# Kernel optimization log

Hardware: AMD Instinct MI355X
Metric: run time of the kernel (lower is better)

## Reference

```python
import jax, jax.numpy as jnp
import numpy as np
from jax import lax

SCALE = 1.0
SHIFT = 0.0
H = 1024
IN = 1024
B = 64
S = 512


def setup_inputs() -> dict:
    key = jax.random.key(0)
    ks = jax.random.split(key, 9)
    s_in = 1.0 / np.sqrt(IN)
    s_h = 1.0 / np.sqrt(H)
    return {
        "x": jax.random.normal(ks[0], (B, S, IN), jnp.float32),
        # layer 0: ih Linear(IN, 4H), hh Linear(H, 4H) — torch stores W as [out, in]
        "W_ih0": jax.random.uniform(ks[1], (4 * H, IN), jnp.float32, -s_in, s_in),
        "b_ih0": jax.random.uniform(ks[2], (4 * H,), jnp.float32, -s_in, s_in),
        "W_hh0": jax.random.uniform(ks[3], (4 * H, H), jnp.float32, -s_h, s_h),
        "b_hh0": jax.random.uniform(ks[4], (4 * H,), jnp.float32, -s_h, s_h),
        # layer 1: ih Linear(H, 4H), hh Linear(H, 4H)
        "W_ih1": jax.random.uniform(ks[5], (4 * H, H), jnp.float32, -s_h, s_h),
        "b_ih1": jax.random.uniform(ks[6], (4 * H,), jnp.float32, -s_h, s_h),
        "W_hh1": jax.random.uniform(ks[7], (4 * H, H), jnp.float32, -s_h, s_h),
        "b_hh1": jax.random.uniform(ks[8], (4 * H,), jnp.float32, -s_h, s_h),
    }


def _scaled_sigmoid(x):
    return SCALE * jax.nn.sigmoid(x) + SHIFT


def _lstm_layer(x_seq, W_ih, b_ih, W_hh, b_hh):
    """x_seq: (B, S, D). Returns (outputs (B,S,H), h_n (B,H), c_n (B,H))."""
    b = x_seq.shape[0]
    # precompute input projections for all timesteps: (S, B, 4H)
    xp = (jnp.einsum('bsd,gd->sbg', x_seq, W_ih) + b_ih).astype(x_seq.dtype)

    def step(carry, xp_t):
        h, c = carry
        gates = xp_t + h @ W_hh.T + b_hh  # (B, 4H)
        i_g, f_g, g_g, o_g = jnp.split(gates, 4, axis=-1)
        i = _scaled_sigmoid(i_g)
        f = _scaled_sigmoid(f_g)
        g = jnp.tanh(g_g)
        o = _scaled_sigmoid(o_g)
        c_next = f * c + i * g
        h_next = o * jnp.tanh(c_next)
        return (h_next, c_next), h_next

    h0 = jnp.zeros((b, W_hh.shape[1]), x_seq.dtype)
    c0 = jnp.zeros((b, W_hh.shape[1]), x_seq.dtype)
    (h_n, c_n), ys = lax.scan(step, (h0, c0), xp)
    return ys.transpose(1, 0, 2), h_n, c_n


def reference(x, W_ih0, b_ih0, W_hh0, b_hh0, W_ih1, b_ih1, W_hh1, b_hh1):
    out0, h0, c0 = _lstm_layer(x, W_ih0, b_ih0, W_hh0, b_hh0)
    out1, h1, c1 = _lstm_layer(out0, W_ih1, b_ih1, W_hh1, b_hh1)
    h_n = jnp.stack([h0, h1], axis=0)  # (num_layers, B, H)
    c_n = jnp.stack([c0, c1], axis=0)
    return out1, h_n, c_n
```

## Files before the change

### kernel.cpp

```cpp
#include <hip/hip_runtime.h>
#include <stdint.h>

typedef __attribute__((ext_vector_type(8))) short short8;
typedef __attribute__((ext_vector_type(4))) float f32x4;

#define MFMA16(a, b, c) __builtin_amdgcn_mfma_f32_16x16x32_bf16((a), (b), (c), 0, 0, 0)
#define AL(p) __hip_atomic_load((p), __ATOMIC_RELAXED, __HIP_MEMORY_SCOPE_AGENT)
#define AS(p, v) __hip_atomic_store((p), (v), __ATOMIC_RELAXED, __HIP_MEMORY_SCOPE_AGENT)

__device__ __forceinline__ unsigned short f2bf(float f) {
  unsigned u = __float_as_uint(f);
  u = (u + 0x7FFFu + ((u >> 16) & 1u)) >> 16;
  return (unsigned short)u;
}
__device__ __forceinline__ float bf2f(unsigned short u) {
  return __uint_as_float(((unsigned)u) << 16);
}

__global__ void k_prep(const float* __restrict__ x,
                       const float* __restrict__ w0, const float* __restrict__ w1,
                       const float* __restrict__ w2, const float* __restrict__ w3,
                       const float* __restrict__ a0, const float* __restrict__ b0,
                       const float* __restrict__ a1, const float* __restrict__ b1,
                       unsigned short* __restrict__ xbf,
                       unsigned short* __restrict__ wbf,
                       float* __restrict__ bias0, float* __restrict__ bias1) {
  const int gid = blockIdx.x * blockDim.x + threadIdx.x;
  const int stride = gridDim.x * blockDim.x;
  for (int i = gid; i < 8192; i += stride) {
    if (i < 4096) bias0[i] = a0[i] + b0[i];
    else          bias1[i - 4096] = a1[i - 4096] + b1[i - 4096];
  }
  for (int i = gid; i < 8388608; i += stride) {
    float4 v = reinterpret_cast<const float4*>(x)[i];
    ushort4 o;
    o.x = f2bf(v.x); o.y = f2bf(v.y); o.z = f2bf(v.z); o.w = f2bf(v.w);
    reinterpret_cast<ushort4*>(xbf)[i] = o;
  }
  for (int i = gid; i < 4194304; i += stride) {
    const float* sp = (i < 1048576) ? w0 : (i < 2097152) ? w1
                     : (i < 3145728) ? w2 : w3;
    float4 v = reinterpret_cast<const float4*>(sp)[i & 1048575];
    ushort4 o;
    o.x = f2bf(v.x); o.y = f2bf(v.y); o.z = f2bf(v.z); o.w = f2bf(v.w);
    reinterpret_cast<ushort4*>(wbf)[i] = o;
  }
}

__global__ __launch_bounds__(256) void k_gemm(
    const unsigned short* __restrict__ A,
    const unsigned short* __restrict__ W,
    const float* __restrict__ bias,
    unsigned short* __restrict__ out,
    int mode) {
  __shared__ unsigned short trs[128 * 128];
  const int tid = threadIdx.x, l = tid & 63, wv = tid >> 6;
  const int wm = wv >> 1, wn = wv & 1;
  const int tm = blockIdx.x >> 5, tn = blockIdx.x & 31;
  const int m_base = tm * 128 + wm * 64;
  const int jc0 = tn << 5;
  const int lr = l & 15, k8 = (l >> 4) << 3;

  size_t a_off[4], b_off[4];
#pragma unroll
  for (int i = 0; i < 4; ++i) {
    int r = m_base + i * 16 + lr;
    int ar = mode ? r : (((r & 63) << 9) + (r >> 6));
    a_off[i] = ((size_t)ar << 10) + k8;
    int ct = (wn << 6) + i * 16 + lr;
    int wrow = ((ct >> 5) << 10) + jc0 + (ct & 31);
    b_off[i] = ((size_t)wrow << 10) + k8;
  }
  f32x4 acc[4][4] = {};
#pragma unroll 2
  for (int k0 = 0; k0 < 1024; k0 += 32) {
    short8 a[4], b[4];
#pragma unroll
    for (int i = 0; i < 4; ++i) a[i] = *reinterpret_cast<const short8*>(A + a_off[i] + k0);
#pragma unroll
    for (int j = 0; j < 4; ++j) b[j] = *reinterpret_cast<const short8*>(W + b_off[j] + k0);
#pragma unroll
    for (int i = 0; i < 4; ++i)
#pragma unroll
      for (int j = 0; j < 4; ++j) acc[i][j] = MFMA16(a[i], b[j], acc[i][j]);
  }
  const int oq = (l >> 4) << 2, oc = l & 15;
#pragma unroll
  for (int j = 0; j < 4; ++j) {
    int ct = (wn << 6) + j * 16 + oc;
    int gate = ct >> 5, jl = ct & 31;
    float bs = bias[(gate << 10) + jc0 + jl];
#pragma unroll
    for (int i = 0; i < 4; ++i) {
      int rt = (wm << 6) + i * 16 + oq;
#pragma unroll
      for (int q = 0; q < 4; ++q)
        trs[((rt + q) << 7) + (jl << 2) + gate] = f2bf(acc[i][j][q] + bs);
    }
  }
  __syncthreads();
#pragma unroll
  for (int s = 0; s < 8; ++s) {
    int ch = tid + (s << 8);
    int row = ch >> 4, off16 = (ch & 15) << 3;
    short8 v = *reinterpret_cast<const short8*>(trs + (ch << 3));
    *reinterpret_cast<short8*>(
        out + (((size_t)(m_base - (wm << 6) + row)) << 12) + (jc0 << 2) + off16) = v;
  }
}

__device__ __forceinline__ void gemm_chunk(
    const unsigned short* __restrict__ out0,
    const unsigned short* __restrict__ Wih1,
    const float* __restrict__ bias1,
    unsigned short* __restrict__ xb,
    const int* __restrict__ gf0,
    int* __restrict__ gmin_lds,
    char* smem, int g, int hc0, int c,
    int tid, int l, int ks, int lr16, int k8) {
  const int cg = (ks << 4) + lr16;
  const int gate = cg >> 5, jl = cg & 31;
  const int wrow = (gate << 10) + hc0 + jl;
  const float bsv = bias1[wrow];
  unsigned short* trs = (unsigned short*)smem;

  int gmin = 0;
  for (int mb = 0; mb < 16; ++mb) {
    const int thr = (c << 6) + (mb << 2) + 5;
    if (gmin < thr) {
      if (tid == 0) {
        int m;
        for (;;) {
          m = 0x7fffffff;
          for (int i = 0; i < 32; ++i) { int f = AL(&gf0[i]); m = (f < m) ? f : m; }
          if (m >= thr) break;
          __builtin_amdgcn_s_sleep(4);
        }
        *gmin_lds = m;
      }
      __syncthreads();
      gmin = *gmin_lds;
    }

    f32x4 acc[4] = {{0.f,0.f,0.f,0.f},{0.f,0.f,0.f,0.f},{0.f,0.f,0.f,0.f},{0.f,0.f,0.f,0.f}};
#pragma unroll 1
    for (int kh = 0; kh < 2; ++kh) {
      short8 st[8];
#pragma unroll
      for (int s = 0; s < 8; ++s) {
        int ch = tid + (s << 9);
        int row = ch >> 6, kc = ch & 63;
        int t = (c << 6) + (mb << 2) + (row >> 4);
        int b = (g << 4) + (row & 15);
        st[s] = *reinterpret_cast<const short8*>(
            out0 + (((size_t)((t << 6) + b)) << 10) + (kh << 9) + (kc << 3));
      }
#pragma unroll
      for (int s = 0; s < 8; ++s) {
        int ch = tid + (s << 9);
        int row = ch >> 6, kc = ch & 63;
        *reinterpret_cast<short8*>(smem + (row << 10) + ((kc ^ (row & 7)) << 4)) = st[s];
      }
      __syncthreads();
#pragma unroll
      for (int kk = 0; kk < 16; ++kk) {
        short8 bfr = *reinterpret_cast<const short8*>(
            Wih1 + ((size_t)wrow << 10) + (kh << 9) + (kk << 5) + k8);
        int kc = (kk << 2) + (k8 >> 3);
#pragma unroll
        for (int mt = 0; mt < 4; ++mt) {
          int row = (mt << 4) + lr16;
          short8 a = *reinterpret_cast<const short8*>(
              smem + (row << 10) + ((kc ^ (row & 7)) << 4));
          acc[mt] = MFMA16(a, bfr, acc[mt]);
        }
      }
      __syncthreads();
    }
#pragma unroll
    for (int mt = 0; mt < 4; ++mt)
#pragma unroll
      for (int q = 0; q < 4; ++q) {
        int bi = ((l >> 4) << 2) + q;
        trs[(((mt << 4) + bi) << 7) + (jl << 2) + gate] = f2bf(acc[mt][q] + bsv);
      }
    __syncthreads();
#pragma unroll
    for (int s = 0; s < 2; ++s) {
      int ch = (tid << 1) + s;
      short8 v = *reinterpret_cast<const short8*>(trs + (ch << 3));
      unsigned short* dst = xb + (mb << 13) + (ch << 3);
      asm volatile("global_store_dwordx4 %0, %1, off sc0 sc1"
                   :: "v"(dst), "v"(v) : "memory");
    }
    __syncthreads();
  }
  asm volatile("s_waitcnt vmcnt(0)" ::: "memory");
  __syncthreads();
}

__device__ __forceinline__ void rec0_body(
    const unsigned short* __restrict__ xp,
    const unsigned short* __restrict__ Whh,
    unsigned short* __restrict__ hbuf,
    int* __restrict__ gflags,
    unsigned short* __restrict__ out_bf,
    float* __restrict__ hn, float* __restrict__ cn,
    const unsigned short* __restrict__ Wih1,
    const float* __restrict__ bias1,
    unsigned short* __restrict__ xpp_partner,
    const int* __restrict__ pflag1,
    int* __restrict__ fx_self,
    float* part, int* gmin_lds, int w, int g) {
  const int tid = threadIdx.x;
  const int l = tid & 63, ks = tid >> 6;
  const int hc0 = w << 5;
  const int lr16 = l & 15, k8 = (l >> 4) << 3;

  short8 bf[8][4];
#pragma unroll
  for (int nn = 0; nn < 8; ++nn) {
    const int c_wg = (nn << 4) + lr16;
    const unsigned short* wp =
        Whh + ((size_t)(((c_wg >> 5) << 10) + hc0 + (c_wg & 31)) << 10) + (ks << 7) + k8;
#pragma unroll
    for (int kk = 0; kk < 4; ++kk)
      bf[nn][kk] = *reinterpret_cast<const short8*>(wp + (kk << 5));
  }

  const int arow = (g << 4) + lr16;
  const size_t aoff = ((size_t)arow << 10) + (ks << 7) + k8;

  const int b_l = tid >> 5;
  const int j = tid & 31;
  const int b_g = (g << 4) + b_l;
  const int hcol = hc0 + j;

  float cs = 0.f;

  auto xload = [&](int t) -> uint2 {
    return *reinterpret_cast<const uint2*>(
        xp + (((size_t)((t << 6) + b_g)) << 12) + (hcol << 2));
  };

  auto step = [&](int t, uint2 xv) {
    if (t > 0) {
      const unsigned short* ab = hbuf + ((size_t)(t & 1) << 16) + aoff;
      short8 av[4];
#pragma unroll
      for (int kk = 0; kk < 4; ++kk) {
        const unsigned short* p = ab + (kk << 5);
        asm volatile("global_load_dwordx4 %0, %1, off sc0 sc1"
                     : "=v"(av[kk]) : "v"(p) : "memory");
      }
      asm volatile("s_waitcnt vmcnt(0)" ::: "memory");
      __builtin_amdgcn_sched_barrier(0);
      f32x4 acc[8] = {{0.f,0.f,0.f,0.f},{0.f,0.f,0.f,0.f},{0.f,0.f,0.f,0.f},{0.f,0.f,0.f,0.f},
                      {0.f,0.f,0.f,0.f},{0.f,0.f,0.f,0.f},{0.f,0.f,0.f,0.f},{0.f,0.f,0.f,0.f}};
#pragma unroll
      for (int kk = 0; kk < 4; ++kk)
#pragma unroll
        for (int nn = 0; nn < 8; ++nn)
          acc[nn] = MFMA16(av[kk], bf[nn][kk], acc[nn]);
#pragma unroll
      for (int nn = 0; nn < 8; ++nn)
#pragma unroll
        for (int q = 0; q < 4; ++q) {
          int bq = ((l >> 4) << 2) + q;
          part[(((ks << 4) + bq) << 7) + (nn << 4) + lr16] = acc[nn][q];
        }
    }
    __syncthreads();

    float hv, cv;
    unsigned short h16;
    {
      float gi = bf2f((unsigned short)(xv.x)), gf = bf2f((unsigned short)(xv.x >> 16));
      float gg = bf2f((unsigned short)(xv.y)), go = bf2f((unsigned short)(xv.y >> 16));
      if (t > 0) {
        float si = 0.f, sf = 0.f, sg = 0.f, so = 0.f;
#pragma unroll
        for (int ksx = 0; ksx < 8; ++ksx) {
          const float* p = part + (((ksx << 4) + b_l) << 7) + j;
          si += p[0]; sf += p[32]; sg += p[64]; so += p[96];
        }
        gi += si; gf += sf; gg += sg; go += so;
      }
      float iv = 1.f / (1.f + __expf(-gi));
      float fv = 1.f / (1.f + __expf(-gf));
      float gv = tanhf(gg);
      float ov = 1.f / (1.f + __expf(-go));
      cs = fv * cs + iv * gv;
      hv = ov * tanhf(cs);
      cv = cs;
      h16 = f2bf(hv);
      AS(hbuf + ((size_t)((t + 1) & 1) << 16) + ((size_t)b_g << 10) + hcol, h16);
    }
    asm volatile("s_waitcnt vmcnt(0)" ::: "memory");
    __syncthreads();
    if (tid == 0) AS(&gflags[w], t + 1);

    AS(out_bf + ((((size_t)t << 6) + b_g) << 10) + hcol, h16);
    if (t == 511) {
      hn[((size_t)b_g << 10) + hcol] = hv;
      cn[((size_t)b_g << 10) + hcol] = cv;
    } else {
      const int base = ks << 2;
      for (;;) {
        int f = (l < 4) ? AL(&gflags[base + l]) : 0x7fffffff;
        if (__all(f > t)) break;
        __builtin_amdgcn_s_sleep(1);
      }
    }
  };

  uint2 zz = {0u, 0u};
  uint2 xA[4] = {zz, zz, zz, zz}, xB[4] = {zz, zz, zz, zz};
#pragma unroll
  for (int s = 0; s < 4; ++s) xA[s] = xload(s);
  for (int tc = 0; tc < 512; tc += 8) {
#pragma unroll
    for (int s = 0; s < 4; ++s) xB[s] = xload(tc + 4 + s);
#pragma unroll
    for (int s = 0; s < 4; ++s) step(tc + s, xA[s]);
    if (tc + 8 < 512) {
#pragma unroll
      for (int s = 0; s < 4; ++s) xA[s] = xload(tc + 8 + s);
    }
#pragma unroll
    for (int s = 0; s < 4; ++s) step(tc + 4 + s, xB[s]);
  }

  asm volatile("s_waitcnt vmcnt(0)" ::: "memory");
  __syncthreads();
  if (tid == 0) AS(&gflags[w], 1000);

  if (tid == 0) {
    for (;;) {
      bool ok = true;
      for (int i = 0; i < 32; ++i)
        if (AL(&gflags[i]) < 1000) { ok = false; break; }
      if (ok) break;
      __builtin_amdgcn_s_sleep(16);
    }
  }
  __syncthreads();
  for (int c = 5; c < 8; ++c) {
    const int need = (c - 1) << 6;
    if (tid == 0) {
      while (AL(pflag1) < need) __builtin_amdgcn_s_sleep(16);
    }
    __syncthreads();
    gemm_chunk(out_bf, Wih1, bias1,
               xpp_partner + ((size_t)(c & 1) << 17),
               gflags, gmin_lds,
               (char*)part, g, hc0, c, tid, l, ks, lr16, k8);
    if (tid == 0) AS(fx_self, c + 1);
  }
}

__device__ __forceinline__ void layer1_body(
    const unsigned short* __restrict__ out0,
    const unsigned short* __restrict__ Wih1,
    const float* __restrict__ bias1,
    const unsigned short* __restrict__ Whh1,
    unsigned short* __restrict__ xpp,
    unsigned short* __restrict__ hbuf,
    int* __restrict__ gflags0,
    int* __restrict__ gflags1,
    const int* __restrict__ fx_self,
    float* __restrict__ outf,
    float* __restrict__ hn, float* __restrict__ cn,
    float* part, int* gmin_lds, int u, int g) {
  const int tid = threadIdx.x;
  const int l = tid & 63, ks = tid >> 6;
  const int hc0 = u << 5;
  const int lr16 = l & 15, k8 = (l >> 4) << 3;

  short8 bf[8][4];
#pragma unroll
  for (int nn = 0; nn < 8; ++nn) {
    const int c_wg = (nn << 4) + lr16;
    const unsigned short* wp =
        Whh1 + ((size_t)(((c_wg >> 5) << 10) + hc0 + (c_wg & 31)) << 10) + (ks << 7) + k8;
#pragma unroll
    for (int kk = 0; kk < 4; ++kk)
      bf[nn][kk] = *reinterpret_cast<const short8*>(wp + (kk << 5));
  }

  const int arow = (g << 4) + lr16;
  const size_t aoff = ((size_t)arow << 10) + (ks << 7) + k8;
  const int b_l = tid >> 5, j = tid & 31;
  const int b_g = (g << 4) + b_l;
  const int hcol = hc0 + j;

  float cs = 0.f;

  for (int c = 0; c < 8; ++c) {
    if (c < 5) {
      gemm_chunk(out0, Wih1, bias1,
                 xpp + ((size_t)(c & 1) << 17),
                 gflags0, gmin_lds,
                 (char*)part, g, hc0, c, tid, l, ks, lr16, k8);
    } else {
      if (tid == 0) {
        while (AL(fx_self) < c + 1) __builtin_amdgcn_s_sleep(16);
      }
      __syncthreads();
    }

    const unsigned short* xb = xpp + ((size_t)(c & 1) << 17);
    for (int ti = 0; ti < 64; ++ti) {
      const int t = (c << 6) + ti;
      uint2 xv;
      {
        const unsigned short* p = xb + (((ti << 4) + b_l) << 7) + (j << 2);
        asm volatile("global_load_dwordx2 %0, %1, off sc0 sc1"
                     : "=v"(xv) : "v"(p) : "memory");
      }

      if (t > 0) {
        const unsigned short* ab = hbuf + ((size_t)(t & 1) << 16) + aoff;
        short8 av[4];
#pragma unroll
        for (int kk = 0; kk < 4; ++kk) {
          const unsigned short* p = ab + (kk << 5);
          asm volatile("global_load_dwordx4 %0, %1, off sc0 sc1"
                       : "=v"(av[kk]) : "v"(p) : "memory");
        }
        asm volatile("s_waitcnt vmcnt(0)" ::: "memory");
        __builtin_amdgcn_sched_barrier(0);
        f32x4 acc[8] = {{0.f,0.f,0.f,0.f},{0.f,0.f,0.f,0.f},{0.f,0.f,0.f,0.f},{0.f,0.f,0.f,0.f},
                        {0.f,0.f,0.f,0.f},{0.f,0.f,0.f,0.f},{0.f,0.f,0.f,0.f},{0.f,0.f,0.f,0.f}};
#pragma unroll
        for (int kk = 0; kk < 4; ++kk)
#pragma unroll
          for (int nn = 0; nn < 8; ++nn)
            acc[nn] = MFMA16(av[kk], bf[nn][kk], acc[nn]);
#pragma unroll
        for (int nn = 0; nn < 8; ++nn)
#pragma unroll
          for (int q = 0; q < 4; ++q) {
            int bq = ((l >> 4) << 2) + q;
            part[(((ks << 4) + bq) << 7) + (nn << 4) + lr16] = acc[nn][q];
          }
      } else {
        asm volatile("s_waitcnt vmcnt(0)" ::: "memory");
      }
      __syncthreads();

      float hv, cv;
      unsigned short h16;
      {
        float gi = bf2f((unsigned short)(xv.x)), gf = bf2f((unsigned short)(xv.x >> 16));
        float gg = bf2f((unsigned short)(xv.y)), go = bf2f((unsigned short)(xv.y >> 16));
        if (t > 0) {
          float si = 0.f, sf = 0.f, sg = 0.f, so = 0.f;
#pragma unroll
          for (int ksx = 0; ksx < 8; ++ksx) {
            const float* p = part + (((ksx << 4) + b_l) << 7) + j;
            si += p[0]; sf += p[32]; sg += p[64]; so += p[96];
          }
          gi += si; gf += sf; gg += sg; go += so;
        }
        float iv = 1.f / (1.f + __expf(-gi));
        float fv = 1.f / (1.f + __expf(-gf));
        float gv = tanhf(gg);
        float ov = 1.f / (1.f + __expf(-go));
        cs = fv * cs + iv * gv;
        hv = ov * tanhf(cs);
        cv = cs;
        h16 = f2bf(hv);
        AS(hbuf + ((size_t)((t + 1) & 1) << 16) + ((size_t)b_g << 10) + hcol, h16);
      }
      asm volatile("s_waitcnt vmcnt(0)" ::: "memory");
      __syncthreads();
      if (tid == 0) AS(&gflags1[u], t + 1);

      outf[((((size_t)b_g << 9) + t) << 10) + hcol] = hv;
      if (t == 511) {
        hn[((size_t)b_g << 10) + hcol] = hv;
        cn[((size_t)b_g << 10) + hcol] = cv;
      } else {
        const int base = ks << 2;
        for (;;) {
          int f = (l < 4) ? AL(&gflags1[base + l]) : 0x7fffffff;
          if (__all(f > t)) break;
          __builtin_amdgcn_s_sleep(1);
        }
      }
    }
  }
}

__global__ __launch_bounds__(512, 2) void k_fused(
    const unsigned short* __restrict__ xp0,
    const unsigned short* __restrict__ Whh0,
    unsigned short* __restrict__ hb0,
    int* __restrict__ flags0,
    unsigned short* __restrict__ out0,
    float* __restrict__ hn, float* __restrict__ cn,
    const unsigned short* __restrict__ Wih1,
    const float* __restrict__ bias1,
    const unsigned short* __restrict__ Whh1,
    unsigned short* __restrict__ xpp_all,
    unsigned short* __restrict__ hb1,
    int* __restrict__ flags1,
    int* __restrict__ fx,
    float* __restrict__ outf) {
  __shared__ float part[8 * 16 * 128];
  __shared__ int gmin;
  const int wg = blockIdx.x;
  if (wg < 128) {
    rec0_body(xp0, Whh0, hb0, flags0 + ((wg >> 5) << 8), out0, hn, cn,
              Wih1, bias1,
              xpp_all + ((size_t)wg << 18),
              &flags1[((wg >> 5) << 8) + (wg & 31)],
              &fx[wg],
              part, &gmin, wg & 31, wg >> 5);
  } else {
    const int w1 = wg - 128;
    layer1_body(out0, Wih1, bias1, Whh1,
                xpp_all + ((size_t)w1 << 18),
                hb1, flags0 + ((w1 >> 5) << 8), flags1 + ((w1 >> 5) << 8),
                &fx[w1],
                outf, hn + 65536, cn + 65536,
                part, &gmin, w1 & 31, w1 >> 5);
  }
}

extern "C" void kernel_launch(void* const* d_in, const int* in_sizes, int n_in,
                              void* d_out, int out_size, void* d_ws, size_t ws_size,
                              hipStream_t stream) {
  (void)in_sizes; (void)n_in; (void)out_size; (void)ws_size;
  const float* x    = (const float*)d_in[0];
  const float* Wih0 = (const float*)d_in[1];
  const float* bih0 = (const float*)d_in[2];
  const float* Whh0 = (const float*)d_in[3];
  const float* bhh0 = (const float*)d_in[4];
  const float* Wih1 = (const float*)d_in[5];
  const float* bih1 = (const float*)d_in[6];
  const float* Whh1 = (const float*)d_in[7];
  const float* bhh1 = (const float*)d_in[8];
  float* dout = (float*)d_out;

  char* ws = (char*)d_ws;
  int*            flags0 = (int*)ws;
  int*            flags1 = (int*)(ws + 4096);
  int*            fx     = (int*)(ws + 8192);
  unsigned short* hb0    = (unsigned short*)(ws + 12288);
  unsigned short* hb1    = (unsigned short*)(ws + 274432);
  float*          bias0  = (float*)(ws + 536576);
  float*          bias1  = (float*)(ws + 552960);
  unsigned short* wbf    = (unsigned short*)(ws + 569344);
  unsigned short* xbf    = wbf + 16777216;
  unsigned short* out0   = xbf + 33554432;
  unsigned short* xpb    = out0 + 33554432;

  hipMemsetAsync(flags0, 0, 12288, stream);

  k_prep<<<2048, 256, 0, stream>>>(x, Wih0, Whh0, Wih1, Whh1,
                                   bih0, bhh0, bih1, bhh1,
                                   xbf, wbf, bias0, bias1);

  float* hn = dout + 33554432;
  float* cn = dout + 33554432 + 131072;

  k_gemm<<<8192, 256, 0, stream>>>(xbf, wbf + 0, bias0, xpb, 0);

  k_fused<<<256, 512, 0, stream>>>(xpb, wbf + 4194304, hb0, flags0,
                                   out0, hn, cn,
                                   wbf + 8388608, bias1, wbf + 12582912,
                                   xbf, hb1, flags1, fx, dout);
}
```

Before: 4.027 ms.

## Stage GEMM tiles through XOR-swizzled LDS instead of direct global fragment loads

The input-projection GEMM kernel now cooperatively loads 128x64 A and W tiles into shared memory with an XOR swizzle, then each wave reads its MFMA fragments from LDS. Before, every wave fetched its own fragments straight from global memory, so neighbouring waves loaded the same rows twice. The new scheme is meant to cut global traffic and keep LDS reads free of bank conflicts. It adds two barriers per K step and has no double buffering, so global load latency is no longer overlapped with compute.

New measurement: 3.521 ms. 12.6% less time.

```diff
diff --git a/kernel.cpp b/kernel.cpp
--- a/kernel.cpp
+++ b/kernel.cpp
@@ -53,37 +53,69 @@
     const float* __restrict__ bias,
     unsigned short* __restrict__ out,
     int mode) {
-  __shared__ unsigned short trs[128 * 128];
+  __shared__ char smem[32768];
+  unsigned short* trs = (unsigned short*)smem;
+  char* bufA = smem;
+  char* bufB = smem + 16384;
+
   const int tid = threadIdx.x, l = tid & 63, wv = tid >> 6;
   const int wm = wv >> 1, wn = wv & 1;
   const int tm = blockIdx.x >> 5, tn = blockIdx.x & 31;
-  const int m_base = tm * 128 + wm * 64;
+  const int mb0 = tm << 7;
   const int jc0 = tn << 5;
-  const int lr = l & 15, k8 = (l >> 4) << 3;
-
-  size_t a_off[4], b_off[4];
-#pragma unroll
-  for (int i = 0; i < 4; ++i) {
-    int r = m_base + i * 16 + lr;
+  const int lr = l & 15;
+  const int c4 = l >> 4;
+
+  size_t sgA[4], sgB[4];
+  int slds[4];
+#pragma unroll
+  for (int s = 0; s < 4; ++s) {
+    int ch = tid + (s << 8);
+    int row = ch >> 3, kc8 = ch & 7;
+    int r = mb0 + row;
     int ar = mode ? r : (((r & 63) << 9) + (r >> 6));
-    a_off[i] = ((size_t)ar << 10) + k8;
-    int ct = (wn << 6) + i * 16 + lr;
-    int wrow = ((ct >> 5) << 10) + jc0 + (ct & 31);
-    b_off[i] = ((size_t)wrow << 10) + k8;
-  }
+    sgA[s] = ((size_t)ar << 10) + ((kc8 ^ (row & 7)) << 3);
+    int wrow = ((row >> 5) << 10) + jc0 + (row & 31);
+    sgB[s] = ((size_t)wrow << 10) + ((kc8 ^ (row & 7)) << 3);
+    slds[s] = ch << 4;
+  }
+
   f32x4 acc[4][4] = {};
-#pragma unroll 2
-  for (int k0 = 0; k0 < 1024; k0 += 32) {
-    short8 a[4], b[4];
-#pragma unroll
-    for (int i = 0; i < 4; ++i) a[i] = *reinterpret_cast<const short8*>(A + a_off[i] + k0);
-#pragma unroll
-    for (int j = 0; j < 4; ++j) b[j] = *reinterpret_cast<const short8*>(W + b_off[j] + k0);
-#pragma unroll
-    for (int i = 0; i < 4; ++i)
-#pragma unroll
-      for (int j = 0; j < 4; ++j) acc[i][j] = MFMA16(a[i], b[j], acc[i][j]);
-  }
+  for (int k0 = 0; k0 < 1024; k0 += 64) {
+    short8 stA[4], stB[4];
+#pragma unroll
+    for (int s = 0; s < 4; ++s) {
+      stA[s] = *reinterpret_cast<const short8*>(A + sgA[s] + k0);
+      stB[s] = *reinterpret_cast<const short8*>(W + sgB[s] + k0);
+    }
+#pragma unroll
+    for (int s = 0; s < 4; ++s) {
+      *reinterpret_cast<short8*>(bufA + slds[s]) = stA[s];
+      *reinterpret_cast<short8*>(bufB + slds[s]) = stB[s];
+    }
+    __syncthreads();
+#pragma unroll
+    for (int kkk = 0; kkk < 2; ++kkk) {
+      short8 a[4], b[4];
+      const int c = (kkk << 2) + c4;
+#pragma unroll
+      for (int i = 0; i < 4; ++i) {
+        int rt = (wm << 6) + (i << 4) + lr;
+        a[i] = *reinterpret_cast<const short8*>(
+            bufA + (rt << 7) + ((c ^ (rt & 7)) << 4));
+        int ct = (wn << 6) + (i << 4) + lr;
+        b[i] = *reinterpret_cast<const short8*>(
+            bufB + (ct << 7) + ((c ^ (ct & 7)) << 4));
+      }
+#pragma unroll
+      for (int i = 0; i < 4; ++i)
+#pragma unroll
+        for (int j = 0; j < 4; ++j)
+          acc[i][j] = MFMA16(a[i], b[j], acc[i][j]);
+    }
+    __syncthreads();
+  }
+
   const int oq = (l >> 4) << 2, oc = l & 15;
 #pragma unroll
   for (int j = 0; j < 4; ++j) {
@@ -105,7 +137,7 @@
     int row = ch >> 4, off16 = (ch & 15) << 3;
     short8 v = *reinterpret_cast<const short8*>(trs + (ch << 3));
     *reinterpret_cast<short8*>(
-        out + (((size_t)(m_base - (wm << 6) + row)) << 12) + (jc0 << 2) + off16) = v;
+        out + (((size_t)(mb0 + row)) << 12) + (jc0 << 2) + off16) = v;
   }
 }
 
```
